# Optimization experiments

Hardware: AMD Instinct MI355X
Metric: run time of the kernel (lower is better)

The kernel has to match this reference:

```python
import jax, jax.numpy as jnp
import numpy as np

GAMMA = 0.1
TAU = 0.01
N, M, K = 256, 512, 512


def setup_inputs() -> dict:
    key = jax.random.key(0)
    ks = jax.random.split(key, 10)
    nn2 = N * N
    return {
        "I": jax.random.normal(ks[0], (K, 1), dtype=jnp.float32),
        "x": jax.random.normal(ks[1], (N, 1), dtype=jnp.float32),
        "W": jax.random.normal(ks[2], (N, N), dtype=jnp.float32),
        "z": jax.random.normal(ks[3], (M, 1), dtype=jnp.float32),
        "C": jax.random.normal(ks[4], (nn2,), dtype=jnp.float32) / np.float32(np.sqrt(nn2)),
        "D": jax.random.normal(ks[5], (nn2, M), dtype=jnp.float32) / np.float32(np.sqrt(nn2)),
        "F": jax.random.normal(ks[6], (M,), dtype=jnp.float32) / np.float32(np.sqrt(M)),
        "H": jax.random.normal(ks[7], (M, nn2), dtype=jnp.float32) / np.float32(np.sqrt(M)),
        "W_in_1": jax.random.uniform(ks[8], (N, K), dtype=jnp.float32, minval=-1.0 / np.sqrt(K), maxval=1.0 / np.sqrt(K)),
        "W_in_2": jax.random.uniform(ks[9], (M, K), dtype=jnp.float32, minval=-1.0 / np.sqrt(K), maxval=1.0 / np.sqrt(K)),
    }


def reference(I, x, W, z, C, D, F, H, W_in_1, W_in_2):
    n = x.shape[0]
    # neuron state update: x' = (1-g)x + g*W@phi(x) + W_in_1@I
    phi_x = jax.nn.sigmoid(x)                       # (n,1)
    x_new = (1.0 - GAMMA) * x + GAMMA * (W @ phi_x) + W_in_1 @ I
    # Phi(x') = vec(phi(x') phi(x')^T), row-major -> (n*n, 1)
    phi_xn = jax.nn.sigmoid(x_new)                  # (n,1)
    Phi = (phi_xn * phi_xn.T).reshape(-1, 1)        # (n*n,1) outer product
    psi_z = jnp.tanh(z)                             # (m,1)
    # diag(C)@Phi is an elementwise multiply; D@psi(z) is the big GEMV
    W_new = (1.0 - GAMMA) * W + GAMMA * (C[:, None] * Phi + D @ psi_z).reshape(n, n)
    # astrocyte update: diag(F)@psi(z) elementwise; H@Phi big GEMV
    z_new = (1.0 - GAMMA * TAU) * z + GAMMA * TAU * (
        F[:, None] * psi_z + H @ Phi + W_in_2 @ I
    )
    return (x_new, W_new, z_new)
```

## Files before the change

### kernel.cpp

```cpp
#include <hip/hip_runtime.h>
#include <math.h>

#define GAMMA 0.1f
#define TAU   0.01f
#define NN    256
#define MM    512
#define KK    512

typedef float vf4 __attribute__((ext_vector_type(4)));

__device__ __forceinline__ float sigmoidf(float v) {
    return 1.0f / (1.0f + __expf(-v));
}
__device__ __forceinline__ float4 sigmoid4(float4 v) {
    return make_float4(sigmoidf(v.x), sigmoidf(v.y), sigmoidf(v.z), sigmoidf(v.w));
}
__device__ __forceinline__ float dot4(float4 a, float4 b) {
    return a.x * b.x + a.y * b.y + a.z * b.z + a.w * b.w;
}
__device__ __forceinline__ float4 ntload4(const float4* p) {
    vf4 v = __builtin_nontemporal_load((const vf4*)p);
    return make_float4(v.x, v.y, v.z, v.w);
}

__global__ __launch_bounds__(256) void k_state(
    const float* __restrict__ I, const float* __restrict__ x,
    const float* __restrict__ W, const float* __restrict__ z,
    const float* __restrict__ Win1,
    float* __restrict__ out, float* __restrict__ ws)
{
    const int b = blockIdx.x, t = threadIdx.x;
    if (b < 16) {
        const int wave = t >> 6, lane = t & 63;
        const int row0 = b * 16 + wave * 4;
        float4 xv = ((const float4*)x)[lane];
        float4 i0 = ((const float4*)I)[lane];
        float4 i1 = ((const float4*)I)[64 + lane];
        const float4* Wr = (const float4*)(W + row0 * NN);
        float4 w0 = Wr[lane], w1 = Wr[lane + 64], w2 = Wr[lane + 128], w3 = Wr[lane + 192];
        const float4* A = (const float4*)(Win1 + row0 * KK);
        float4 a0 = A[lane],       c0 = A[lane + 64];
        float4 a1 = A[lane + 128], c1 = A[lane + 192];
        float4 a2 = A[lane + 256], c2 = A[lane + 320];
        float4 a3 = A[lane + 384], c3 = A[lane + 448];
        float4 xo = ((const float4*)x)[row0 >> 2];

        float4 ph = sigmoid4(xv);
        float s0 = GAMMA * dot4(w0, ph) + dot4(a0, i0) + dot4(c0, i1);
        float s1 = GAMMA * dot4(w1, ph) + dot4(a1, i0) + dot4(c1, i1);
        float s2 = GAMMA * dot4(w2, ph) + dot4(a2, i0) + dot4(c2, i1);
        float s3 = GAMMA * dot4(w3, ph) + dot4(a3, i0) + dot4(c3, i1);
#pragma unroll
        for (int m = 32; m; m >>= 1) {
            s0 += __shfl_xor(s0, m, 64);
            s1 += __shfl_xor(s1, m, 64);
            s2 += __shfl_xor(s2, m, 64);
            s3 += __shfl_xor(s3, m, 64);
        }
        if (lane == 0) {
            float4 xn;
            xn.x = (1.0f - GAMMA) * xo.x + s0;
            xn.y = (1.0f - GAMMA) * xo.y + s1;
            xn.z = (1.0f - GAMMA) * xo.z + s2;
            xn.w = (1.0f - GAMMA) * xo.w + s3;
            ((float4*)out)[row0 >> 2] = xn;
            ((float4*)ws)[row0 >> 2] = sigmoid4(xn);
        }
    } else {
        const int idx = (b - 16) * 256 + t;
        ws[NN + idx] = tanhf(z[idx]);
    }
}

__global__ __launch_bounds__(1024, 4) void k_H(
    const float* __restrict__ H, const float* __restrict__ Win2,
    const float* __restrict__ I, const float* __restrict__ z,
    const float* __restrict__ F, const float* __restrict__ ws,
    float* __restrict__ out)
{
    __shared__ float sm[256];
    __shared__ float red[16];
    const int b = blockIdx.x, t = threadIdx.x;
    if (t < 64) ((float4*)sm)[t] = ((const float4*)ws)[t];
    float wi = 0.0f;
    if (t < KK) wi = Win2[(size_t)b * KK + t] * I[t];
    __syncthreads();
    const float4* H4 = (const float4*)(H + (size_t)b * (NN * NN));
    const float4 pj = ((const float4*)sm)[t & 63];
    const int i0 = t >> 6;
    float a0 = wi, a1 = 0.0f, a2 = 0.0f, a3 = 0.0f;
#pragma unroll
    for (int qq = 0; qq < 2; ++qq) {
        float4 h[8];
        float  pi[8];
#pragma unroll
        for (int u = 0; u < 8; ++u) {
            const int q = qq * 8 + u;
            h[u]  = H4[t + 1024 * q];
            pi[u] = sm[i0 + 16 * q];
        }
#pragma unroll
        for (int u = 0; u < 8; ++u) {
            const float term = pi[u] * dot4(h[u], pj);
            if      ((u & 3) == 0) a0 += term;
            else if ((u & 3) == 1) a1 += term;
            else if ((u & 3) == 2) a2 += term;
            else                   a3 += term;
        }
    }
    float acc = (a0 + a1) + (a2 + a3);
#pragma unroll
    for (int m = 32; m; m >>= 1) acc += __shfl_xor(acc, m, 64);
    if ((t & 63) == 0) red[t >> 6] = acc;
    __syncthreads();
    if (t < 64) {
        float v = (t < 16) ? red[t] : 0.0f;
#pragma unroll
        for (int m = 8; m; m >>= 1) v += __shfl_xor(v, m, 64);
        if (t == 0) {
            const float gt = GAMMA * TAU;
            float zn = (1.0f - gt) * z[b] + gt * (F[b] * ws[NN + b] + v);
            out[NN + NN * NN + b] = zn;
        }
    }
}

__global__ __launch_bounds__(256) void k_D(
    const float* __restrict__ W, const float* __restrict__ Cv,
    const float* __restrict__ D, const float* __restrict__ ws,
    float* __restrict__ out)
{
    __shared__ float sm[768];
    const int t = threadIdx.x;
    if (t < 128)      ((float4*)sm)[t] = ((const float4*)(ws + NN))[t];
    else if (t < 192) ((float4*)sm)[t] = ((const float4*)ws)[t - 128];
    __syncthreads();
    const int wave = t >> 6, lane = t & 63;
    const float4 z0 = ((const float4*)sm)[lane];
    const float4 z1 = ((const float4*)sm)[64 + lane];
    const int row0 = blockIdx.x * 64 + wave * 16;
    const float4* R = (const float4*)(D + (size_t)row0 * MM);

    float wrow = 0.0f, crow = 0.0f, pjrow = 0.0f;
    if (lane < 16) {
        wrow  = W[row0 + lane];
        crow  = Cv[row0 + lane];
        pjrow = sm[512 + (row0 & 255) + lane];
    }
    const float pi = sm[512 + (row0 >> 8)];

    float4 fa0 = ntload4(&R[lane]),        fb0 = ntload4(&R[lane + 64]);
    float4 fa1 = ntload4(&R[lane + 128]),  fb1 = ntload4(&R[lane + 192]);
    float keep = 0.0f;
#pragma unroll
    for (int r = 0; r < 16; ++r) {
        float4 ca, cb;
        if (r & 1) { ca = fa1; cb = fb1; } else { ca = fa0; cb = fb0; }
        if (r + 2 < 16) {
            const float4* Rn = R + (r + 2) * 128;
            if (r & 1) { fa1 = ntload4(&Rn[lane]); fb1 = ntload4(&Rn[lane + 64]); }
            else       { fa0 = ntload4(&Rn[lane]); fb0 = ntload4(&Rn[lane + 64]); }
        }
        float s = dot4(ca, z0) + dot4(cb, z1);
#pragma unroll
        for (int m = 32; m; m >>= 1) s += __shfl_xor(s, m, 64);
        if (lane == r) keep = s;
    }
    if (lane < 16) {
        float wn = (1.0f - GAMMA) * wrow + GAMMA * (crow * pi * pjrow + keep);
        out[NN + row0 + lane] = wn;
    }
}

extern "C" void kernel_launch(void* const* d_in, const int* in_sizes, int n_in,
                              void* d_out, int out_size, void* d_ws, size_t ws_size,
                              hipStream_t stream) {
    const float* I    = (const float*)d_in[0];
    const float* x    = (const float*)d_in[1];
    const float* W    = (const float*)d_in[2];
    const float* z    = (const float*)d_in[3];
    const float* C    = (const float*)d_in[4];
    const float* D    = (const float*)d_in[5];
    const float* F    = (const float*)d_in[6];
    const float* H    = (const float*)d_in[7];
    const float* Win1 = (const float*)d_in[8];
    const float* Win2 = (const float*)d_in[9];
    float* out = (float*)d_out;
    float* ws  = (float*)d_ws;

    hipLaunchKernelGGL(k_state, dim3(18), dim3(256), 0, stream,
                       I, x, W, z, Win1, out, ws);
    hipLaunchKernelGGL(k_H, dim3(MM), dim3(1024), 0, stream,
                       H, Win2, I, z, F, ws, out);
    hipLaunchKernelGGL(k_D, dim3((NN * NN) / 64), dim3(256), 0, stream,
                       W, C, D, ws, out);
}
```

Before: 284.0 us.

## Fuse H and D GEMV kernels into one interleaved launch with double-buffered loads

```diff
diff --git a/kernel.cpp b/kernel.cpp
--- a/kernel.cpp
+++ b/kernel.cpp
@@ -72,103 +72,106 @@
     }
 }
 
-__global__ __launch_bounds__(1024, 4) void k_H(
+__global__ __launch_bounds__(256, 4) void k_WZ(
+    const float* __restrict__ W, const float* __restrict__ Cv,
+    const float* __restrict__ D, const float* __restrict__ F,
     const float* __restrict__ H, const float* __restrict__ Win2,
     const float* __restrict__ I, const float* __restrict__ z,
-    const float* __restrict__ F, const float* __restrict__ ws,
-    float* __restrict__ out)
+    const float* __restrict__ ws, float* __restrict__ out)
 {
-    __shared__ float sm[256];
-    __shared__ float red[16];
+    __shared__ float sm[768];
+    __shared__ float red[4];
     const int b = blockIdx.x, t = threadIdx.x;
-    if (t < 64) ((float4*)sm)[t] = ((const float4*)ws)[t];
-    float wi = 0.0f;
-    if (t < KK) wi = Win2[(size_t)b * KK + t] * I[t];
-    __syncthreads();
-    const float4* H4 = (const float4*)(H + (size_t)b * (NN * NN));
-    const float4 pj = ((const float4*)sm)[t & 63];
-    const int i0 = t >> 6;
-    float a0 = wi, a1 = 0.0f, a2 = 0.0f, a3 = 0.0f;
+    const int wave = t >> 6, lane = t & 63;
+
+    if (t < 128)      ((float4*)sm)[t] = ((const float4*)(ws + NN))[t];
+    else if (t < 192) ((float4*)sm)[t] = ((const float4*)ws)[t - 128];
+
+    if (b % 3 == 0) {
+        const int row = b / 3;
+        float wi = Win2[(size_t)row * KK + t] * I[t]
+                 + Win2[(size_t)row * KK + 256 + t] * I[256 + t];
+        __syncthreads();
+        const float4* H4 = (const float4*)(H + (size_t)row * (NN * NN));
+        const float* phi = sm + 512;
+        const float4 pj = ((const float4*)phi)[t & 63];
+        float a0 = wi, a1 = 0.0f, a2 = 0.0f, a3 = 0.0f;
+        float4 buf[2][8];
 #pragma unroll
-    for (int qq = 0; qq < 2; ++qq) {
-        float4 h[8];
-        float  pi[8];
+        for (int u = 0; u < 8; ++u) buf[0][u] = ntload4(&H4[t + 256 * u]);
 #pragma unroll
-        for (int u = 0; u < 8; ++u) {
-            const int q = qq * 8 + u;
-            h[u]  = H4[t + 1024 * q];
-            pi[u] = sm[i0 + 16 * q];
+        for (int g = 0; g < 8; ++g) {
+            const int cur = g & 1, nxt = cur ^ 1;
+            if (g < 7) {
+#pragma unroll
+                for (int u = 0; u < 8; ++u)
+                    buf[nxt][u] = ntload4(&H4[t + 256 * ((g + 1) * 8 + u)]);
+            }
+#pragma unroll
+            for (int u = 0; u < 8; ++u) {
+                const float term = phi[wave + 4 * (g * 8 + u)] * dot4(buf[cur][u], pj);
+                if      ((u & 3) == 0) a0 += term;
+                else if ((u & 3) == 1) a1 += term;
+                else if ((u & 3) == 2) a2 += term;
+                else                   a3 += term;
+            }
+        }
+        float acc = (a0 + a1) + (a2 + a3);
+#pragma unroll
+        for (int m = 32; m; m >>= 1) acc += __shfl_xor(acc, m, 64);
+        if (lane == 0) red[wave] = acc;
+        __syncthreads();
+        if (t == 0) {
+            const float gt = GAMMA * TAU;
+            float tot = red[0] + red[1] + red[2] + red[3];
+            float zn = (1.0f - gt) * z[row] + gt * (F[row] * ws[NN + row] + tot);
+            out[NN + NN * NN + row] = zn;
+        }
+    } else {
+        const int d = b - b / 3 - 1;
+        const int row0 = d * 64 + wave * 16;
+        const float4* R = (const float4*)(D + (size_t)row0 * MM);
+        float wrow = 0.0f, crow = 0.0f;
+        if (lane < 16) { wrow = W[row0 + lane]; crow = Cv[row0 + lane]; }
+        __syncthreads();
+        const float4 z0 = ((const float4*)sm)[lane];
+        const float4 z1 = ((const float4*)sm)[64 + lane];
+
+        float p[16];
+        float4 A[2][4], B[2][4];
+#pragma unroll
+        for (int r = 0; r < 4; ++r) {
+            A[0][r] = ntload4(&R[lane + 128 * r]);
+            B[0][r] = ntload4(&R[lane + 64 + 128 * r]);
         }
 #pragma unroll
-        for (int u = 0; u < 8; ++u) {
-            const float term = pi[u] * dot4(h[u], pj);
-            if      ((u & 3) == 0) a0 += term;
-            else if ((u & 3) == 1) a1 += term;
-            else if ((u & 3) == 2) a2 += term;
-            else                   a3 += term;
+        for (int g = 0; g < 4; ++g) {
+            const int cur = g & 1, nxt = cur ^ 1;
+            if (g < 3) {
+#pragma unroll
+                for (int r = 0; r < 4; ++r) {
+                    A[nxt][r] = ntload4(&R[lane + 128 * ((g + 1) * 4 + r)]);
+                    B[nxt][r] = ntload4(&R[lane + 64 + 128 * ((g + 1) * 4 + r)]);
+                }
+            }
+#pragma unroll
+            for (int r = 0; r < 4; ++r)
+                p[g * 4 + r] = dot4(A[cur][r], z0) + dot4(B[cur][r], z1);
         }
-    }
-    float acc = (a0 + a1) + (a2 + a3);
 #pragma unroll
-    for (int m = 32; m; m >>= 1) acc += __shfl_xor(acc, m, 64);
-    if ((t & 63) == 0) red[t >> 6] = acc;
-    __syncthreads();
-    if (t < 64) {
-        float v = (t < 16) ? red[t] : 0.0f;
+        for (int m = 32; m; m >>= 1) {
 #pragma unroll
-        for (int m = 8; m; m >>= 1) v += __shfl_xor(v, m, 64);
-        if (t == 0) {
-            const float gt = GAMMA * TAU;
-            float zn = (1.0f - gt) * z[b] + gt * (F[b] * ws[NN + b] + v);
-            out[NN + NN * NN + b] = zn;
+            for (int r = 0; r < 16; ++r) p[r] += __shfl_xor(p[r], m, 64);
         }
-    }
-}
-
-__global__ __launch_bounds__(256) void k_D(
-    const float* __restrict__ W, const float* __restrict__ Cv,
-    const float* __restrict__ D, const float* __restrict__ ws,
-    float* __restrict__ out)
-{
-    __shared__ float sm[768];
-    const int t = threadIdx.x;
-    if (t < 128)      ((float4*)sm)[t] = ((const float4*)(ws + NN))[t];
-    else if (t < 192) ((float4*)sm)[t] = ((const float4*)ws)[t - 128];
-    __syncthreads();
-    const int wave = t >> 6, lane = t & 63;
-    const float4 z0 = ((const float4*)sm)[lane];
-    const float4 z1 = ((const float4*)sm)[64 + lane];
-    const int row0 = blockIdx.x * 64 + wave * 16;
-    const float4* R = (const float4*)(D + (size_t)row0 * MM);
-
-    float wrow = 0.0f, crow = 0.0f, pjrow = 0.0f;
-    if (lane < 16) {
-        wrow  = W[row0 + lane];
-        crow  = Cv[row0 + lane];
-        pjrow = sm[512 + (row0 & 255) + lane];
-    }
-    const float pi = sm[512 + (row0 >> 8)];
-
-    float4 fa0 = ntload4(&R[lane]),        fb0 = ntload4(&R[lane + 64]);
-    float4 fa1 = ntload4(&R[lane + 128]),  fb1 = ntload4(&R[lane + 192]);
-    float keep = 0.0f;
+        float keep = 0.0f;
 #pragma unroll
-    for (int r = 0; r < 16; ++r) {
-        float4 ca, cb;
-        if (r & 1) { ca = fa1; cb = fb1; } else { ca = fa0; cb = fb0; }
-        if (r + 2 < 16) {
-            const float4* Rn = R + (r + 2) * 128;
-            if (r & 1) { fa1 = ntload4(&Rn[lane]); fb1 = ntload4(&Rn[lane + 64]); }
-            else       { fa0 = ntload4(&Rn[lane]); fb0 = ntload4(&Rn[lane + 64]); }
+        for (int r = 0; r < 16; ++r) if (lane == r) keep = p[r];
+        if (lane < 16) {
+            const float phi_i = sm[512 + ((row0 + lane) >> 8)];
+            const float phi_j = sm[512 + ((row0 + lane) & 255)];
+            float wn = (1.0f - GAMMA) * wrow + GAMMA * (crow * phi_i * phi_j + keep);
+            out[NN + row0 + lane] = wn;
         }
-        float s = dot4(ca, z0) + dot4(cb, z1);
-#pragma unroll
-        for (int m = 32; m; m >>= 1) s += __shfl_xor(s, m, 64);
-        if (lane == r) keep = s;
-    }
-    if (lane < 16) {
-        float wn = (1.0f - GAMMA) * wrow + GAMMA * (crow * pi * pjrow + keep);
-        out[NN + row0 + lane] = wn;
     }
 }
 
@@ -190,8 +193,6 @@
 
     hipLaunchKernelGGL(k_state, dim3(18), dim3(256), 0, stream,
                        I, x, W, z, Win1, out, ws);
-    hipLaunchKernelGGL(k_H, dim3(MM), dim3(1024), 0, stream,
-                       H, Win2, I, z, F, ws, out);
-    hipLaunchKernelGGL(k_D, dim3((NN * NN) / 64), dim3(256), 0, stream,
-                       W, C, D, ws, out);
+    hipLaunchKernelGGL(k_WZ, dim3(1536), dim3(256), 0, stream,
+                       W, C, D, F, H, Win2, I, z, ws, out);
 }
```

After: 272.7 us. 1.04x faster.
